# Kernel optimization log

Measured on AMD Instinct MI355X. Metric: run time of the kernel, lower is better.

The kernel has to match this reference:

```python
import jax, jax.numpy as jnp
import numpy as np

N_NODES = 100000
N_EDGES = 1000000
D_FEAT = 64
N_FILTER = 64
N_CLASSES = 16


def gcn_norm(edge_idx, n):
    """Add self-loops and compute symmetric normalization D^-1/2 (A+I) D^-1/2."""
    loop = jnp.arange(n, dtype=edge_idx.dtype)
    src = jnp.concatenate([edge_idx[0], loop])  # [E+N]
    dst = jnp.concatenate([edge_idx[1], loop])  # [E+N]
    w = jnp.ones(src.shape[0], dtype=jnp.float32)
    deg = jax.ops.segment_sum(w, dst, num_segments=n)  # in-degree incl. self-loop
    dinv = jnp.where(deg > 0, jax.lax.rsqrt(deg), 0.0)
    norm = dinv[src] * w * dinv[dst]  # [E+N]
    return src, dst, norm


def gcn_conv(x, W, b, src, dst, norm, n):
    h = x @ W                                   # [n, f] dense transform first (f <= d)
    msg = h[src] * norm[:, None]                # gather + scale  [E+N, f]
    out = jax.ops.segment_sum(msg, dst, num_segments=n)  # scatter-add  [n, f]
    return out + b


def setup_inputs() -> dict:
    key = jax.random.key(0)
    k1, k2, k3, k4 = jax.random.split(key, 4)
    X = jax.random.normal(k1, (N_NODES, D_FEAT), dtype=jnp.float32)
    edge_idx = jax.random.randint(k2, (2, N_EDGES), 0, N_NODES, dtype=jnp.int64)
    W1 = jax.random.normal(k3, (D_FEAT, N_FILTER), dtype=jnp.float32) * 0.05
    b1 = jnp.zeros((N_FILTER,), dtype=jnp.float32)
    W2 = jax.random.normal(k4, (N_FILTER, N_CLASSES), dtype=jnp.float32) * 0.05
    b2 = jnp.zeros((N_CLASSES,), dtype=jnp.float32)
    return {"X": X, "edge_idx": edge_idx, "W1": W1, "b1": b1, "W2": W2, "b2": b2}


def reference(X, edge_idx, W1, b1, W2, b2):
    n = X.shape[0]
    src, dst, norm = gcn_norm(edge_idx, n)
    x = gcn_conv(X, W1, b1, src, dst, norm, n)
    x = jax.nn.relu(x)
    # dropout p=0 -> identity
    x = gcn_conv(x, W2, b2, src, dst, norm, n)
    return x  # raw logits; pred_layer is not applied in the torch forward
```

## Files before the change

### kernel.cpp

```cpp
#include <hip/hip_runtime.h>
#include <hip/hip_bf16.h>


constexpr int N = 100000;
constexpr int E = 1000000;
constexpr int NB = (N + 511) / 512;
constexpr int CAP = 6144;
constexpr int CSTRIDE = 32;
constexpr int CHUNK = 2048;
constexpr int NBLK = (E + CHUNK - 1) / CHUNK;

__device__ __forceinline__ float rl_f(float v, int l) {
    return __int_as_float(__builtin_amdgcn_readlane(__float_as_int(v), l));
}
__device__ __forceinline__ int rl_i(int v, int l) {
    return __builtin_amdgcn_readlane(v, l);
}
__device__ __forceinline__ float bflo(unsigned u) { return __uint_as_float(u << 16); }
__device__ __forceinline__ float bfhi(unsigned u) { return __uint_as_float(u & 0xffff0000u); }

__global__ void k_bfill(const int* __restrict__ src, const int* __restrict__ dst,
                        int* __restrict__ cursor, int* __restrict__ bkt) {
    __shared__ int hist[256];
    __shared__ int lbase[256];
    __shared__ int gbase[256];
    __shared__ int lcur[256];
    __shared__ int stage[CHUNK];
    __shared__ unsigned char sbkt[CHUNK];
    int t = threadIdx.x;
    int e0 = blockIdx.x * CHUNK;
    int cnt = min(CHUNK, E - e0);

    hist[t] = 0;
    __syncthreads();
    for (int j = t; j < cnt; j += 256)
        atomicAdd(&hist[dst[e0 + j] >> 9], 1);
    __syncthreads();
    int h = hist[t];
    lbase[t] = h;
    __syncthreads();
    for (int off = 1; off < 256; off <<= 1) {
        int x = (t >= off) ? lbase[t - off] : 0;
        __syncthreads();
        lbase[t] += x;
        __syncthreads();
    }
    int excl = lbase[t] - h;
    __syncthreads();
    lbase[t] = excl;
    lcur[t] = 0;
    if (t < NB) gbase[t] = h ? atomicAdd(&cursor[t * CSTRIDE], h) : 0;
    __syncthreads();
    for (int j = t; j < cnt; j += 256) {
        int d = dst[e0 + j];
        int b = d >> 9;
        int pos = lbase[b] + atomicAdd(&lcur[b], 1);
        stage[pos] = ((d & 511) << 17) | src[e0 + j];
        sbkt[pos] = (unsigned char)b;
    }
    __syncthreads();
    for (int j = t; j < cnt; j += 256) {
        int b = sbkt[j];
        int gpos = gbase[b] + (j - lbase[b]);
        if (gpos < CAP) bkt[b * CAP + gpos] = stage[j];
    }
}

__global__ void k_bfine(const int* __restrict__ cursor, const int* __restrict__ bkt,
                        int* __restrict__ row_ptr, float* __restrict__ dinv,
                        int* __restrict__ csr_src) {
    __shared__ int sd[256];
    __shared__ int cnt[512];
    __shared__ int excl[512];
    __shared__ int s2[256];
    int b = blockIdx.x;
    int t = threadIdx.x;
    int c = (t < NB) ? cursor[t * CSTRIDE] : 0;
    sd[t] = c;
    __syncthreads();
    for (int off = 1; off < 256; off <<= 1) {
        int x = (t >= off) ? sd[t - off] : 0;
        __syncthreads();
        sd[t] += x;
        __syncthreads();
    }
    int m = cursor[b * CSTRIDE];
    int base = sd[b] - m;
    if (b == 0 && t == 0) row_ptr[N] = E;
    const int* bb = bkt + b * CAP;
    cnt[t] = 0; cnt[t + 256] = 0;
    __syncthreads();
    for (int j = t; j < m; j += 256) atomicAdd(&cnt[bb[j] >> 17], 1);
    __syncthreads();
    int pairSum = cnt[2 * t] + cnt[2 * t + 1];
    s2[t] = pairSum;
    __syncthreads();
    for (int off = 1; off < 256; off <<= 1) {
        int x = (t >= off) ? s2[t - off] : 0;
        __syncthreads();
        s2[t] += x;
        __syncthreads();
    }
    int exclPair = s2[t] - pairSum;
    excl[2 * t] = exclPair;
    excl[2 * t + 1] = exclPair + cnt[2 * t];
    __syncthreads();
#pragma unroll
    for (int hh = 0; hh < 2; ++hh) {
        int k = t + hh * 256;
        int node = b * 512 + k;
        if (node < N) {
            row_ptr[node] = base + excl[k];
            dinv[node] = rsqrtf((float)(cnt[k] + 1));
        }
    }
    __syncthreads();
    for (int j = t; j < m; j += 256) {
        int v = bb[j];
        int p = atomicAdd(&excl[v >> 17], 1);
        csr_src[base + p] = v & 0x1FFFF;
    }
}

__global__ void k_gemm1(const float* __restrict__ X, const float* __restrict__ W1,
                        const float* __restrict__ dinv, __hip_bfloat16* __restrict__ h1s) {
    int t = threadIdx.x;
    int lane = t & 63;
    int wid = (blockIdx.x * 256 + t) >> 6;
    float w1[64];
#pragma unroll
    for (int k = 0; k < 64; ++k) w1[k] = W1[k * 64 + lane];
    for (int row = wid; row < N; row += 4096) {
        float x = X[(size_t)row * 64 + lane];
        float acc = 0.f;
#pragma unroll
        for (int k = 0; k < 64; ++k) acc = fmaf(rl_f(x, k), w1[k], acc);
        acc *= dinv[row];
        float up = __shfl_xor(acc, 1);
        if (!(lane & 1)) {
            __hip_bfloat162 p;
            p.x = __float2bfloat16(acc);
            p.y = __float2bfloat16(up);
            *(__hip_bfloat162*)(h1s + (size_t)row * 64 + lane) = p;
        }
    }
}

__global__ void k_layer12(const int* __restrict__ row_ptr, const int* __restrict__ csr_src,
                          const float* __restrict__ dinv, const __hip_bfloat16* __restrict__ h1s,
                          const float* __restrict__ b1, const float* __restrict__ W2,
                          __hip_bfloat16* __restrict__ h2s) {
    int t = threadIdx.x;
    int lane = t & 63;
    int g = lane >> 4;
    int q = lane & 15;
    int wid = (blockIdx.x * 256 + t) >> 6;
    float w2[16];
#pragma unroll
    for (int j = 0; j < 16; ++j) w2[j] = W2[(g * 16 + j) * 16 + q];
    float b1v = b1[lane];
    const uint2* H = (const uint2*)h1s;

    for (int d = wid; d < N; d += 8192) {
        int rp0 = row_ptr[d], rp1 = row_ptr[d + 1];
        float dv = dinv[d];
        float a0 = 0.f, a1 = 0.f, a2 = 0.f, a3 = 0.f;
        if (g == 0) {
            uint2 u = H[(size_t)d * 16 + q];
            a0 = bflo(u.x); a1 = bfhi(u.x); a2 = bflo(u.y); a3 = bfhi(u.y);
        }
        for (int base = rp0; base < rp1; base += 64) {
            int nloc = min(64, rp1 - base);
            int sidx = (lane < nloc) ? csr_src[base + lane] : 0;
            int j = 0;
            for (; j + 3 < nloc; j += 4) {
                int s0 = rl_i(sidx, j), s1 = rl_i(sidx, j + 1);
                int s2v = rl_i(sidx, j + 2), s3v = rl_i(sidx, j + 3);
                int sa = (lane & 16) ? s1 : s0;
                int sb = (lane & 16) ? s3v : s2v;
                int sg = (lane & 32) ? sb : sa;
                uint2 u = H[(size_t)sg * 16 + q];
                a0 += bflo(u.x); a1 += bfhi(u.x); a2 += bflo(u.y); a3 += bfhi(u.y);
            }
            for (; j < nloc; ++j) {
                int s = rl_i(sidx, j);
                if (lane < 16) {
                    uint2 u = H[(size_t)s * 16 + q];
                    a0 += bflo(u.x); a1 += bfhi(u.x); a2 += bflo(u.y); a3 += bfhi(u.y);
                }
            }
        }
        a0 += __shfl_xor(a0, 16); a1 += __shfl_xor(a1, 16);
        a2 += __shfl_xor(a2, 16); a3 += __shfl_xor(a3, 16);
        a0 += __shfl_xor(a0, 32); a1 += __shfl_xor(a1, 32);
        a2 += __shfl_xor(a2, 32); a3 += __shfl_xor(a3, 32);
        int srcl = lane >> 2;
        float v0 = __shfl(a0, srcl), v1 = __shfl(a1, srcl);
        float v2 = __shfl(a2, srcl), v3 = __shfl(a3, srcl);
        float ysum = (lane & 2) ? ((lane & 1) ? v3 : v2) : ((lane & 1) ? v1 : v0);
        float y = fmaxf(fmaf(dv, ysum, b1v), 0.f);
        float o = 0.f;
#pragma unroll
        for (int j = 0; j < 16; ++j) o = fmaf(__shfl(y, (lane & 48) | j), w2[j], o);
        o += __shfl_xor(o, 16);
        o += __shfl_xor(o, 32);
        o *= dv;
        float oup = __shfl_xor(o, 1);
        if (lane < 16 && !(lane & 1)) {
            __hip_bfloat162 p;
            p.x = __float2bfloat16(o);
            p.y = __float2bfloat16(oup);
            *(__hip_bfloat162*)(h2s + (size_t)d * 16 + lane) = p;
        }
    }
}

__global__ void k_gather2(const int* __restrict__ row_ptr, const int* __restrict__ csr_src,
                          const float* __restrict__ dinv, const __hip_bfloat16* __restrict__ h2s,
                          const float* __restrict__ b2, float* __restrict__ out) {
    int t = threadIdx.x;
    int lane = t & 63;
    int g = lane >> 3;
    int cp = lane & 7;
    int d = blockIdx.x * 4 + (t >> 6);
    int rp0 = row_ptr[d], rp1 = row_ptr[d + 1];
    float dv = dinv[d];
    const unsigned* H2 = (const unsigned*)h2s;
    float e0 = 0.f, e1 = 0.f;
    if (g == 0) {
        unsigned u = H2[(size_t)d * 8 + cp];
        e0 = bflo(u); e1 = bfhi(u);
    }
    for (int j = rp0 + g; j < rp1; j += 8) {
        int s = csr_src[j];
        unsigned u = H2[(size_t)s * 8 + cp];
        e0 += bflo(u); e1 += bfhi(u);
    }
    e0 += __shfl_xor(e0, 8);  e1 += __shfl_xor(e1, 8);
    e0 += __shfl_xor(e0, 16); e1 += __shfl_xor(e1, 16);
    e0 += __shfl_xor(e0, 32); e1 += __shfl_xor(e1, 32);
    if (lane < 8) {
        float2 r;
        r.x = fmaf(dv, e0, b2[2 * cp]);
        r.y = fmaf(dv, e1, b2[2 * cp + 1]);
        *(float2*)(out + (size_t)d * 16 + 2 * cp) = r;
    }
}

extern "C" void kernel_launch(void* const* d_in, const int* in_sizes, int n_in,
                              void* d_out, int out_size, void* d_ws, size_t ws_size,
                              hipStream_t stream) {
    const float* X  = (const float*)d_in[0];
    const int*   ei = (const int*)d_in[1];
    const float* W1 = (const float*)d_in[2];
    const float* b1 = (const float*)d_in[3];
    const float* W2 = (const float*)d_in[4];
    const float* b2 = (const float*)d_in[5];
    float* out = (float*)d_out;

    int* cursor  = (int*)d_ws;
    int* row_ptr = cursor + NB * CSTRIDE;
    int* bkt     = row_ptr + N + 4;
    int* csr_src = bkt + NB * CAP;
    float* dinv  = (float*)(csr_src + E);
    __hip_bfloat16* h1s = (__hip_bfloat16*)(dinv + N);
    __hip_bfloat16* h2s = h1s + (size_t)N * 64;

    const int* src = ei;
    const int* dst = ei + E;

    hipMemsetAsync(cursor, 0, NB * CSTRIDE * sizeof(int), stream);
    k_bfill<<<NBLK, 256, 0, stream>>>(src, dst, cursor, bkt);
    k_bfine<<<NB, 256, 0, stream>>>(cursor, bkt, row_ptr, dinv, csr_src);
    k_gemm1<<<1024, 256, 0, stream>>>(X, W1, dinv, h1s);
    k_layer12<<<2048, 256, 0, stream>>>(row_ptr, csr_src, dinv, h1s, b1, W2, h2s);
    k_gather2<<<N / 4, 256, 0, stream>>>(row_ptr, csr_src, dinv, h2s, b2, out);
}
```

Baseline: 217.2 us.

## Widen gather loads, assign contiguous node ranges per wave, use zero sentinel rows

Both gather kernels now give each wave a contiguous range of 13 destination nodes. Neighbour rows are gathered with wider vector loads (16 bytes per lane in layer 1, 8 in layer 2), so more edges are in flight per step. A zeroed sentinel row at index N lets padded lanes load harmlessly without branching, and layer-1 partial sums are reduced through LDS instead of shuffles. The edge bucketing chunk is also doubled. These changes aim to raise memory-level parallelism and cut shuffle and tail overhead, at the cost of more register and LDS pressure and possible load imbalance across waves.

After: 213.9 us. No clear change (-1.6%).

```diff
diff --git a/kernel.cpp b/kernel.cpp
--- a/kernel.cpp
+++ b/kernel.cpp
@@ -7,14 +7,14 @@
 constexpr int NB = (N + 511) / 512;
 constexpr int CAP = 6144;
 constexpr int CSTRIDE = 32;
-constexpr int CHUNK = 2048;
+constexpr int CHUNK = 4096;
 constexpr int NBLK = (E + CHUNK - 1) / CHUNK;
+constexpr int NPW = 13;
+constexpr int NW = (N + NPW - 1) / NPW;
+constexpr int NWBLK = (NW + 3) / 4;
 
 __device__ __forceinline__ float rl_f(float v, int l) {
     return __int_as_float(__builtin_amdgcn_readlane(__float_as_int(v), l));
-}
-__device__ __forceinline__ int rl_i(int v, int l) {
-    return __builtin_amdgcn_readlane(v, l);
 }
 __device__ __forceinline__ float bflo(unsigned u) { return __uint_as_float(u << 16); }
 __device__ __forceinline__ float bfhi(unsigned u) { return __uint_as_float(u & 0xffff0000u); }
@@ -123,10 +123,15 @@
 }
 
 __global__ void k_gemm1(const float* __restrict__ X, const float* __restrict__ W1,
-                        const float* __restrict__ dinv, __hip_bfloat16* __restrict__ h1s) {
+                        const float* __restrict__ dinv, __hip_bfloat16* __restrict__ h1s,
+                        __hip_bfloat16* __restrict__ h2s) {
     int t = threadIdx.x;
     int lane = t & 63;
     int wid = (blockIdx.x * 256 + t) >> 6;
+    if (blockIdx.x == 0) {
+        if (t < 64) h1s[(size_t)N * 64 + t] = __float2bfloat16(0.f);
+        if (t < 16) h2s[(size_t)N * 16 + t] = __float2bfloat16(0.f);
+    }
     float w1[64];
 #pragma unroll
     for (int k = 0; k < 64; ++k) w1[k] = W1[k * 64 + lane];
@@ -150,54 +155,53 @@
                           const float* __restrict__ dinv, const __hip_bfloat16* __restrict__ h1s,
                           const float* __restrict__ b1, const float* __restrict__ W2,
                           __hip_bfloat16* __restrict__ h2s) {
+    __shared__ float sy[4][8][72];
     int t = threadIdx.x;
     int lane = t & 63;
-    int g = lane >> 4;
-    int q = lane & 15;
-    int wid = (blockIdx.x * 256 + t) >> 6;
+    int w = t >> 6;
+    int g8 = lane >> 3;
+    int qo = (lane & 7) << 4;
+    int g16 = lane >> 4, c16 = lane & 15;
+    int wid = blockIdx.x * 4 + w;
+    int d0 = wid * NPW;
+    if (d0 >= N) return;
+    int dend = min(d0 + NPW, N);
     float w2[16];
 #pragma unroll
-    for (int j = 0; j < 16; ++j) w2[j] = W2[(g * 16 + j) * 16 + q];
+    for (int j = 0; j < 16; ++j) w2[j] = W2[(g16 * 16 + j) * 16 + c16];
     float b1v = b1[lane];
-    const uint2* H = (const uint2*)h1s;
-
-    for (int d = wid; d < N; d += 8192) {
-        int rp0 = row_ptr[d], rp1 = row_ptr[d + 1];
+    const char* Hb = (const char*)h1s;
+
+    int rp0 = row_ptr[d0];
+    for (int d = d0; d < dend; ++d) {
+        int rp1 = row_ptr[d + 1];
         float dv = dinv[d];
-        float a0 = 0.f, a1 = 0.f, a2 = 0.f, a3 = 0.f;
-        if (g == 0) {
-            uint2 u = H[(size_t)d * 16 + q];
-            a0 = bflo(u.x); a1 = bfhi(u.x); a2 = bflo(u.y); a3 = bfhi(u.y);
+        float a[8] = {0, 0, 0, 0, 0, 0, 0, 0};
+        if (g8 == 0) {
+            uint4 u = *(const uint4*)(Hb + (((unsigned)d << 7) | qo));
+            a[0] = bflo(u.x); a[1] = bfhi(u.x); a[2] = bflo(u.y); a[3] = bfhi(u.y);
+            a[4] = bflo(u.z); a[5] = bfhi(u.z); a[6] = bflo(u.w); a[7] = bfhi(u.w);
         }
         for (int base = rp0; base < rp1; base += 64) {
             int nloc = min(64, rp1 - base);
-            int sidx = (lane < nloc) ? csr_src[base + lane] : 0;
-            int j = 0;
-            for (; j + 3 < nloc; j += 4) {
-                int s0 = rl_i(sidx, j), s1 = rl_i(sidx, j + 1);
-                int s2v = rl_i(sidx, j + 2), s3v = rl_i(sidx, j + 3);
-                int sa = (lane & 16) ? s1 : s0;
-                int sb = (lane & 16) ? s3v : s2v;
-                int sg = (lane & 32) ? sb : sa;
-                uint2 u = H[(size_t)sg * 16 + q];
-                a0 += bflo(u.x); a1 += bfhi(u.x); a2 += bflo(u.y); a3 += bfhi(u.y);
+            int sidx = (lane < nloc) ? csr_src[base + lane] : N;
+            int steps = (nloc + 7) >> 3;
+            for (int j = 0; j < steps; ++j) {
+                int s = __shfl(sidx, (j << 3) | g8);
+                uint4 u = *(const uint4*)(Hb + (((unsigned)s << 7) | qo));
+                a[0] += bflo(u.x); a[1] += bfhi(u.x);
+                a[2] += bflo(u.y); a[3] += bfhi(u.y);
+                a[4] += bflo(u.z); a[5] += bfhi(u.z);
+                a[6] += bflo(u.w); a[7] += bfhi(u.w);
             }
-            for (; j < nloc; ++j) {
-                int s = rl_i(sidx, j);
-                if (lane < 16) {
-                    uint2 u = H[(size_t)s * 16 + q];
-                    a0 += bflo(u.x); a1 += bfhi(u.x); a2 += bflo(u.y); a3 += bfhi(u.y);
-                }
-            }
-        }
-        a0 += __shfl_xor(a0, 16); a1 += __shfl_xor(a1, 16);
-        a2 += __shfl_xor(a2, 16); a3 += __shfl_xor(a3, 16);
-        a0 += __shfl_xor(a0, 32); a1 += __shfl_xor(a1, 32);
-        a2 += __shfl_xor(a2, 32); a3 += __shfl_xor(a3, 32);
-        int srcl = lane >> 2;
-        float v0 = __shfl(a0, srcl), v1 = __shfl(a1, srcl);
-        float v2 = __shfl(a2, srcl), v3 = __shfl(a3, srcl);
-        float ysum = (lane & 2) ? ((lane & 1) ? v3 : v2) : ((lane & 1) ? v1 : v0);
+        }
+        rp0 = rp1;
+        float* row = &sy[w][g8][(lane & 7) << 3];
+        *(float4*)row = make_float4(a[0], a[1], a[2], a[3]);
+        *(float4*)(row + 4) = make_float4(a[4], a[5], a[6], a[7]);
+        __builtin_amdgcn_s_waitcnt(0);
+        float ysum = sy[w][0][lane] + sy[w][1][lane] + sy[w][2][lane] + sy[w][3][lane]
+                   + sy[w][4][lane] + sy[w][5][lane] + sy[w][6][lane] + sy[w][7][lane];
         float y = fmaxf(fmaf(dv, ysum, b1v), 0.f);
         float o = 0.f;
 #pragma unroll
@@ -220,30 +224,54 @@
                           const float* __restrict__ b2, float* __restrict__ out) {
     int t = threadIdx.x;
     int lane = t & 63;
-    int g = lane >> 3;
-    int cp = lane & 7;
-    int d = blockIdx.x * 4 + (t >> 6);
-    int rp0 = row_ptr[d], rp1 = row_ptr[d + 1];
-    float dv = dinv[d];
-    const unsigned* H2 = (const unsigned*)h2s;
-    float e0 = 0.f, e1 = 0.f;
-    if (g == 0) {
-        unsigned u = H2[(size_t)d * 8 + cp];
-        e0 = bflo(u); e1 = bfhi(u);
-    }
-    for (int j = rp0 + g; j < rp1; j += 8) {
-        int s = csr_src[j];
-        unsigned u = H2[(size_t)s * 8 + cp];
-        e0 += bflo(u); e1 += bfhi(u);
-    }
-    e0 += __shfl_xor(e0, 8);  e1 += __shfl_xor(e1, 8);
-    e0 += __shfl_xor(e0, 16); e1 += __shfl_xor(e1, 16);
-    e0 += __shfl_xor(e0, 32); e1 += __shfl_xor(e1, 32);
-    if (lane < 8) {
-        float2 r;
-        r.x = fmaf(dv, e0, b2[2 * cp]);
-        r.y = fmaf(dv, e1, b2[2 * cp + 1]);
-        *(float2*)(out + (size_t)d * 16 + 2 * cp) = r;
+    int g4 = lane >> 2;
+    int q2 = lane & 3;
+    int qo = q2 << 3;
+    int wid = blockIdx.x * 4 + (t >> 6);
+    int d0 = wid * NPW;
+    if (d0 >= N) return;
+    int dend = min(d0 + NPW, N);
+    float b2v[4];
+#pragma unroll
+    for (int k = 0; k < 4; ++k) b2v[k] = b2[q2 * 4 + k];
+    const char* Hb = (const char*)h2s;
+
+    int rp0 = row_ptr[d0];
+    for (int d = d0; d < dend; ++d) {
+        int rp1 = row_ptr[d + 1];
+        float dv = dinv[d];
+        float a[4] = {0, 0, 0, 0};
+        if (g4 == 0) {
+            uint2 u = *(const uint2*)(Hb + (((unsigned)d << 5) | qo));
+            a[0] = bflo(u.x); a[1] = bfhi(u.x); a[2] = bflo(u.y); a[3] = bfhi(u.y);
+        }
+        for (int base = rp0; base < rp1; base += 64) {
+            int nloc = min(64, rp1 - base);
+            int sidx = (lane < nloc) ? csr_src[base + lane] : N;
+            int steps = (nloc + 15) >> 4;
+            for (int j = 0; j < steps; ++j) {
+                int s = __shfl(sidx, (j << 4) | g4);
+                uint2 u = *(const uint2*)(Hb + (((unsigned)s << 5) | qo));
+                a[0] += bflo(u.x); a[1] += bfhi(u.x);
+                a[2] += bflo(u.y); a[3] += bfhi(u.y);
+            }
+        }
+        rp0 = rp1;
+#pragma unroll
+        for (int k = 0; k < 4; ++k) {
+            a[k] += __shfl_xor(a[k], 4);
+            a[k] += __shfl_xor(a[k], 8);
+            a[k] += __shfl_xor(a[k], 16);
+            a[k] += __shfl_xor(a[k], 32);
+        }
+        if (lane < 4) {
+            float4 r;
+            r.x = fmaf(dv, a[0], b2v[0]);
+            r.y = fmaf(dv, a[1], b2v[1]);
+            r.z = fmaf(dv, a[2], b2v[2]);
+            r.w = fmaf(dv, a[3], b2v[3]);
+            *(float4*)(out + (size_t)d * 16 + q2 * 4) = r;
+        }
     }
 }
 
@@ -264,7 +292,7 @@
     int* csr_src = bkt + NB * CAP;
     float* dinv  = (float*)(csr_src + E);
     __hip_bfloat16* h1s = (__hip_bfloat16*)(dinv + N);
-    __hip_bfloat16* h2s = h1s + (size_t)N * 64;
+    __hip_bfloat16* h2s = h1s + (size_t)(N + 1) * 64;
 
     const int* src = ei;
     const int* dst = ei + E;
@@ -272,7 +300,7 @@
     hipMemsetAsync(cursor, 0, NB * CSTRIDE * sizeof(int), stream);
     k_bfill<<<NBLK, 256, 0, stream>>>(src, dst, cursor, bkt);
     k_bfine<<<NB, 256, 0, stream>>>(cursor, bkt, row_ptr, dinv, csr_src);
-    k_gemm1<<<1024, 256, 0, stream>>>(X, W1, dinv, h1s);
-    k_layer12<<<2048, 256, 0, stream>>>(row_ptr, csr_src, dinv, h1s, b1, W2, h2s);
-    k_gather2<<<N / 4, 256, 0, stream>>>(row_ptr, csr_src, dinv, h2s, b2, out);
-}
+    k_gemm1<<<1024, 256, 0, stream>>>(X, W1, dinv, h1s, h2s);
+    k_layer12<<<NWBLK, 256, 0, stream>>>(row_ptr, csr_src, dinv, h1s, b1, W2, h2s);
+    k_gather2<<<NWBLK, 256, 0, stream>>>(row_ptr, csr_src, dinv, h2s, b2, out);
+}
```
